# Performance work log

Hardware: AMD Instinct MI355X
Metric: run time of the kernel (lower is better)

The kernel has to match this reference:

```python
import jax, jax.numpy as jnp
import numpy as np

NUM_CLASSES = 21
TOP_K = 200
CONF_THRESH = 0.01
NMS_THRESH = 0.045
VAR0, VAR1 = 0.1, 0.2  # SSD decode variances
B, N = 128, 8732  # batch, num anchors (SSD300)


def setup_inputs() -> dict:
    key = jax.random.key(0)
    k1, k2, k3 = jax.random.split(key, 3)
    loc = jax.random.normal(k1, (B, N, 4), jnp.float32)
    conf = jax.random.normal(k2, (B, N, NUM_CLASSES), jnp.float32)
    # anchors in center-size form (cx, cy, w, h), values in (0,1)
    anchors = jax.random.uniform(k3, (N, 4), jnp.float32)
    return {"loc": loc, "conf": conf, "anchors": anchors}


def decode(loc, anchors):
    # loc [N,4], anchors [N,4] (cx,cy,w,h) -> corner boxes [N,4]
    cxcy = anchors[:, :2] + loc[:, :2] * VAR0 * anchors[:, 2:]
    wh = anchors[:, 2:] * jnp.exp(loc[:, 2:] * VAR1)
    return jnp.concatenate([cxcy - 0.5 * wh, cxcy + 0.5 * wh], axis=-1)


def pairwise_iou(boxes):
    # boxes [K,4] -> IoU [K,K]
    lt = jnp.maximum(boxes[:, None, :2], boxes[None, :, :2])
    rb = jnp.minimum(boxes[:, None, 2:], boxes[None, :, 2:])
    wh = jnp.clip(rb - lt, 0.0)
    inter = wh[..., 0] * wh[..., 1]
    area = (boxes[:, 2] - boxes[:, 0]) * (boxes[:, 3] - boxes[:, 1])
    return inter / (area[:, None] + area[None, :] - inter + 1e-12)


def nms_one_class(scores, boxes):
    # scores [N], boxes [N,4] -> packed [TOP_K, 5] (score, x1,y1,x2,y2)
    masked = jnp.where(scores > CONF_THRESH, scores, 0.0)
    top_s, idx = jax.lax.top_k(masked, TOP_K)
    top_b = boxes[idx]                      # [K,4]
    iou = pairwise_iou(top_b)               # [K,K]
    ar = jnp.arange(TOP_K)
    def body(i, keep):
        sup = keep[i] & (iou[i] > NMS_THRESH) & (ar > i)
        return keep & ~sup
    keep = jax.lax.fori_loop(0, TOP_K, body, top_s > CONF_THRESH)
    # pack kept detections to the front (stable sort preserves score order)
    order = jnp.argsort(jnp.logical_not(keep))
    ent = jnp.concatenate([top_s[:, None], top_b], axis=-1)[order]
    return jnp.where(keep[order][:, None], ent, 0.0)


def reference(loc, conf, anchors):
    probs = jax.nn.softmax(conf, axis=-1)   # [B,N,C]
    def per_image(loc_i, probs_i):
        boxes = decode(loc_i, anchors)      # [N,4]
        return jax.vmap(lambda s: nms_one_class(s, boxes))(probs_i.T)  # [C,K,5]
    out = jax.vmap(per_image)(loc, probs)   # [B,C,K,5]
    return out.at[:, 0].set(0.0)            # class 0 = background, left zero
```

## Files before the change

kernel.cpp:

```cpp
#include <hip/hip_runtime.h>
#include <math.h>

#pragma clang fp contract(off)

#define NB 128
#define NA 8732
#define NAP 8736
#define NC 21
#define TOPK 200
#define BCAP 512
#define CONF_T 0.01
#define NMS_T 0.045
#define NV (NAP / 8)
#define HSIZE 904
#define CHN 226
#define CHPAD 232
#define CH2N 29
#define KSAMP 30

__device__ __forceinline__ double exact_score_cf(const float* __restrict__ conf,
                                                 int b, int i, int c) {
  const float* row = conf + ((size_t)b * NA + i) * NC;
  float r[NC];
#pragma unroll
  for (int k = 0; k < NC; ++k) r[k] = row[k];
  float mx = r[0];
#pragma unroll
  for (int k = 1; k < NC; ++k) mx = fmaxf(mx, r[k]);
  double d = 0.0;
#pragma unroll
  for (int k = 0; k < NC; ++k) d += exp((double)r[k] - (double)mx);
  double s = exp((double)r[c] - (double)mx) / d;
  return (s > CONF_T) ? s : 0.0;
}

__device__ __forceinline__ double exact_score_aux(const float* __restrict__ conf,
                                                  const double2* __restrict__ aux,
                                                  int b, int i, int c) {
  size_t r = (size_t)b * NA + i;
  double v = (double)conf[r * NC + c];
  double2 a = aux[r];
  double s = exp(v - a.y) / a.x;
  return (s > CONF_T) ? s : 0.0;
}

__device__ __forceinline__ double exact_score(const float* __restrict__ conf,
                                              const double2* __restrict__ aux,
                                              int use_aux, int b, int i, int c) {
  if (use_aux) return exact_score_aux(conf, aux, b, i, c);
  return exact_score_cf(conf, b, i, c);
}

__device__ __forceinline__ void decode64(const float* __restrict__ loc,
                                         const float* __restrict__ anchors,
                                         int b, int ai, double* o) {
  const float* lp = loc + ((size_t)b * NA + ai) * 4;
  const float* ap = anchors + (size_t)ai * 4;
  double l0 = (double)lp[0], l1 = (double)lp[1];
  double l2 = (double)lp[2], l3 = (double)lp[3];
  double a0 = (double)ap[0], a1 = (double)ap[1];
  double a2 = (double)ap[2], a3 = (double)ap[3];
  double cx = a0 + (l0 * 0.1) * a2;
  double cy = a1 + (l1 * 0.1) * a3;
  double w = a2 * exp(l2 * 0.2);
  double h = a3 * exp(l3 * 0.2);
  o[0] = cx - 0.5 * w; o[1] = cy - 0.5 * h;
  o[2] = cx + 0.5 * w; o[3] = cy + 0.5 * h;
}

__device__ __forceinline__ bool entBefore(double sa, int ia, double sb, int ib) {
  return (sa > sb) || (sa == sb && ia < ib);
}

__device__ __forceinline__ unsigned wave_suffix_sum(unsigned v, int lane) {
#pragma unroll
  for (int off = 1; off < 64; off <<= 1) {
    unsigned o = (unsigned)__shfl_down((int)v, off);
    v += (lane + off < 64) ? o : 0u;
  }
  return v;
}

__global__ __launch_bounds__(256) void k_prep(const float* __restrict__ conf,
                                              unsigned short* __restrict__ scores,
                                              double2* __restrict__ aux,
                                              int do_aux) {
  __shared__ float rows[256 * NC];
  int base = blockIdx.x * 256;
  const float4* src = (const float4*)(conf + (size_t)base * NC);
  float4* dst = (float4*)rows;
  for (int t = threadIdx.x; t < (256 * NC) / 4; t += 256) dst[t] = src[t];
  __syncthreads();
  int g = base + threadIdx.x;
  const float* row = rows + threadIdx.x * NC;
  float v[NC];
#pragma unroll
  for (int k = 0; k < NC; ++k) v[k] = row[k];
  float mx = v[0];
#pragma unroll
  for (int k = 1; k < NC; ++k) mx = fmaxf(mx, v[k]);
  float e[NC], s = 0.0f;
#pragma unroll
  for (int k = 0; k < NC; ++k) {
    e[k] = expf(v[k] - mx);
    s += e[k];
  }
  float inv = 1.0f / s;
  int b = g / NA, i = g - b * NA;
#pragma unroll
  for (int cc = 1; cc < NC; ++cc) {
    float sc = e[cc] * inv;
    scores[(size_t)(b * (NC - 1) + (cc - 1)) * NAP + i] =
        (sc > 0.0099f) ? (unsigned short)(__float_as_uint(sc) >> 16)
                       : (unsigned short)0;
  }
  if (do_aux) {
    double d = 0.0;
#pragma unroll
    for (int k = 0; k < NC; ++k) d += exp((double)v[k] - (double)mx);
    aux[g] = make_double2(d, (double)mx);
  }
}

__global__ __launch_bounds__(256) void k_pad(unsigned short* __restrict__ scores,
                                             float* __restrict__ out) {
  int t = blockIdx.x * 256 + threadIdx.x;
  if (t < NB * TOPK * 5) {
    int bb = t / (TOPK * 5);
    int r = t - bb * (TOPK * 5);
    out[(size_t)bb * NC * TOPK * 5 + r] = 0.0f;
  }
  if (t < NB * (NC - 1)) {
    unsigned short* p = scores + (size_t)t * NAP + NA;
    p[0] = 0; p[1] = 0; p[2] = 0; p[3] = 0;
  }
}

__global__ __launch_bounds__(256, 8) void k_fast(const float* __restrict__ loc,
                                                 const float* __restrict__ conf,
                                                 const float* __restrict__ anchors,
                                                 const unsigned short* __restrict__ scores,
                                                 const double2* __restrict__ aux,
                                                 float* __restrict__ out,
                                                 int use_aux) {
  int id = blockIdx.x;
  int xcd = id & 7, slot0 = id >> 3;
  int c = 1 + (slot0 % (NC - 1));
  int b = (slot0 / (NC - 1)) * 8 + xcd;
  int tid = threadIdx.x;
  float* outbase = out + ((size_t)(b * NC + c)) * TOPK * 5;

  __shared__ unsigned hist[HSIZE];
  __shared__ unsigned chunk[CHPAD];
  __shared__ unsigned chunk2[32];
  union U2 {
    struct { double bnds[BCAP]; int bndi[BCAP]; } bb;
    double dbox[TOPK][4];
  };
  __shared__ U2 u2;
  union U3 {
    unsigned suf[HSIZE];
    struct { float4 fbox[TOPK]; float farea[TOPK]; } fb;
  };
  __shared__ U3 u3;
  __shared__ double ssel[256];
  __shared__ int isel[256];
  __shared__ unsigned keepw[7];
  __shared__ int ctl_cnt, ctl_m, ctl_n1, ctl_kneed, ctl_lo, ctl_hi, ctl_k;
  __shared__ int ctl_fix, ctl_redo;
  __shared__ unsigned ctl_pref, ctl_L;

  const unsigned short* srow =
      scores + (size_t)(b * (NC - 1) + (c - 1)) * NAP;
  const uint4* sv = (const uint4*)srow;

  for (int t = tid; t < TOPK; t += 256) isel[t] = 0;
  if (tid < 32) chunk2[tid] = 0u;
  if (tid == 0) { ctl_cnt = 0; ctl_m = 0; ctl_fix = 0; }
  __syncthreads();
  {
    unsigned k16 = srow[tid * 34];
    if (k16) {
      int x = (int)k16 - 0x3BFF;
      if (x < 1) x = 1;
      if (x > HSIZE - 1) x = HSIZE - 1;
      atomicAdd(&chunk2[x >> 5], 1u);
    }
  }
  __syncthreads();
  if (tid < 64) {
    unsigned h = (tid < CH2N) ? chunk2[tid] : 0u;
    unsigned s = wave_suffix_sum(h, tid);
    unsigned long long bal = __ballot((int)(tid < CH2N && s >= (unsigned)KSAMP));
    if (tid == 0) {
      int w = bal ? (63 - (int)__clzll(bal)) : -1;
      ctl_L = (w >= 1) ? (unsigned)(0x3BFF + (w << 5)) : 0u;
    }
  }
  __syncthreads();

  unsigned L16x = ctl_L ? ctl_L : 1u;
  int lo, hi, n1, kneed;
  for (;;) {
    for (int t = tid; t < HSIZE; t += 256) hist[t] = 0u;
    if (tid == 0) ctl_redo = 0;
    __syncthreads();
    for (int q = tid; q < NV; q += 256) {
      uint4 v = sv[q];
      unsigned ks[8] = {v.x & 0xFFFFu, v.x >> 16, v.y & 0xFFFFu, v.y >> 16,
                        v.z & 0xFFFFu, v.z >> 16, v.w & 0xFFFFu, v.w >> 16};
#pragma unroll
      for (int t = 0; t < 8; ++t) {
        if (ks[t] >= L16x) {
          int x = (int)ks[t] - 0x3BFF;
          if (x < 1) x = 1;
          if (x > HSIZE - 1) x = HSIZE - 1;
          atomicAdd(&hist[x], 1u);
        }
      }
    }
    __syncthreads();
    if (tid < CHN) {
      unsigned csum = 0;
#pragma unroll
      for (int j = 0; j < 4; ++j) csum += hist[tid * 4 + j];
      chunk[tid] = csum;
    } else if (tid < CHPAD) {
      chunk[tid] = 0u;
    }
    __syncthreads();
    if (tid < 64) {
      int lane = tid;
      unsigned h2 = 0;
      if (lane < CH2N) {
        int cb = lane * 8;
#pragma unroll
        for (int j = 0; j < 8; ++j) h2 += chunk[cb + j];
      }
      unsigned s2 = wave_suffix_sum(h2, lane);
      unsigned long long bal = __ballot((int)(lane < CH2N && s2 >= (unsigned)TOPK));
      int t2 = bal ? (63 - (int)__clzll(bal)) : -1;
      if (t2 < 0 && L16x > 1u) {
        if (lane == 0) ctl_redo = 1;
      } else {
        if (t2 < 0) {
          if (lane == 0) {
            ctl_lo = 1; ctl_hi = 0; ctl_n1 = (int)s2; ctl_kneed = TOPK - (int)s2;
          }
        } else {
          unsigned cumS = (unsigned)__shfl((int)(s2 - h2), t2);
          unsigned hc = (lane < 8) ? chunk[t2 * 8 + lane] : 0u;
          unsigned sc = wave_suffix_sum(hc, lane);
          unsigned long long balc =
              __ballot((int)(lane < 8 && cumS + sc >= (unsigned)TOPK));
          int jc = 63 - (int)__clzll(balc);
          int tc = t2 * 8 + jc;
          unsigned cumC = cumS + (unsigned)__shfl((int)(sc - hc), jc);
          unsigned hb = (lane < 4) ? hist[tc * 4 + lane] : 0u;
          unsigned sb = wave_suffix_sum(hb, lane);
          unsigned long long balb =
              __ballot((int)(lane < 4 && cumC + sb >= (unsigned)TOPK));
          int jb = 63 - (int)__clzll(balb);
          int D = tc * 4 + jb;
          unsigned cum = cumC + (unsigned)__shfl((int)(sb - hb), jb);
          int hi_ = (D + 1 < HSIZE) ? D + 1 : D;
          int lo_ = (D - 1 >= 1) ? D - 1 : D;
          unsigned hup = (hi_ > D) ? hist[hi_] : 0u;
          if (lane == 0) {
            ctl_lo = lo_; ctl_hi = hi_;
            ctl_n1 = (int)(cum - hup);
            ctl_kneed = TOPK - ctl_n1;
          }
        }
        if (lane < 32) chunk2[lane] = s2 - h2;
      }
    }
    __syncthreads();
    if (!ctl_redo) break;
    L16x = 1u;
  }
  lo = ctl_lo; hi = ctl_hi; n1 = ctl_n1; kneed = ctl_kneed;

  if (tid < CHN) {
    unsigned s = chunk2[tid >> 3];
    int ge = ((tid >> 3) + 1) << 3;
    for (int u = tid + 1; u < ge; ++u) s += chunk[u];
    int b0 = tid * 4;
    unsigned h3 = hist[b0 + 3], h2 = hist[b0 + 2], h1 = hist[b0 + 1];
    u3.suf[b0 + 3] = s;
    u3.suf[b0 + 2] = s + h3;
    u3.suf[b0 + 1] = s + h3 + h2;
    u3.suf[b0 + 0] = s + h3 + h2 + h1;
  }
  __syncthreads();

  {
    unsigned tC16 = (unsigned)(0x3C00 + hi);
    unsigned tB16 = (unsigned)(0x3BFF + lo);
    for (int q = tid; q < NV; q += 256) {
      uint4 v = sv[q];
      unsigned ks[8] = {v.x & 0xFFFFu, v.x >> 16, v.y & 0xFFFFu, v.y >> 16,
                        v.z & 0xFFFFu, v.z >> 16, v.w & 0xFFFFu, v.w >> 16};
#pragma unroll
      for (int t = 0; t < 8; ++t) {
        unsigned key = ks[t];
        if (key >= tC16) {
          int x = (int)key - 0x3BFF;
          if (x > HSIZE - 1) x = HSIZE - 1;
          int slot = (int)u3.suf[x] + (int)atomicSub(&hist[x], 1u) - 1;
          if (slot < TOPK) isel[slot] = (x << 16) | (q * 8 + t);
        } else if (key >= tB16) {
          int p = atomicAdd(&ctl_m, 1);
          if (p < BCAP) u2.bb.bndi[p] = q * 8 + t;
        }
      }
    }
  }
  __syncthreads();
  int m = (hi > 0) ? ctl_m : 0;

  if (hi > 0 && m > BCAP) {
    if (tid == 0) { ctl_k = TOPK; ctl_pref = 0u; }
    __syncthreads();
    for (int shift = 8; shift >= 0; shift -= 8) {
      hist[tid] = 0u;
      __syncthreads();
      unsigned pref = ctl_pref;
      for (int q = tid; q < NV; q += 256) {
        uint4 v = sv[q];
        unsigned ks[8] = {v.x & 0xFFFFu, v.x >> 16, v.y & 0xFFFFu, v.y >> 16,
                          v.z & 0xFFFFu, v.z >> 16, v.w & 0xFFFFu, v.w >> 16};
#pragma unroll
        for (int t = 0; t < 8; ++t) {
          unsigned key = ks[t];
          if (key == 0u) continue;
          bool match = (shift == 8) || ((key >> 8) == (pref >> 8));
          if (match) atomicAdd(&hist[(key >> shift) & 255u], 1u);
        }
      }
      __syncthreads();
      if (tid == 0) {
        int k = ctl_k;
        unsigned cum = 0;
        int d = 255;
        for (; d > 0; --d) {
          unsigned h = hist[d];
          if (cum + h >= (unsigned)k) break;
          cum += h;
        }
        ctl_k = k - (int)cum;
        ctl_pref = pref | ((unsigned)d << shift);
      }
      __syncthreads();
    }
    unsigned Tf = ctl_pref;
    kneed = ctl_k;
    n1 = TOPK - kneed;
    if (tid == 0) { ctl_cnt = 0; ctl_m = 0; }
    __syncthreads();
    for (int q = tid; q < NV; q += 256) {
      uint4 v = sv[q];
      unsigned ks[8] = {v.x & 0xFFFFu, v.x >> 16, v.y & 0xFFFFu, v.y >> 16,
                        v.z & 0xFFFFu, v.z >> 16, v.w & 0xFFFFu, v.w >> 16};
#pragma unroll
      for (int t = 0; t < 8; ++t) {
        unsigned key = ks[t];
        if (key > Tf) {
          int p = atomicAdd(&ctl_cnt, 1);
          if (p < 256) isel[p] = q * 8 + t;
        } else if (key == Tf) {
          int p = atomicAdd(&ctl_m, 1);
          if (p < BCAP) u2.bb.bndi[p] = q * 8 + t;
        }
      }
    }
    __syncthreads();
    m = ctl_m;
    if (m > BCAP) m = BCAP;
    for (int q = tid; q < m; q += 256)
      u2.bb.bnds[q] = exact_score(conf, aux, use_aux, b, u2.bb.bndi[q], c);
    __syncthreads();
    for (int q = tid; q < m; q += 256) {
      double sq = u2.bb.bnds[q];
      int iq = u2.bb.bndi[q];
      int rank = 0;
      for (int r = 0; r < m; ++r)
        if (entBefore(u2.bb.bnds[r], u2.bb.bndi[r], sq, iq)) ++rank;
      if (rank < kneed) { isel[n1 + rank] = iq; ssel[n1 + rank] = sq; }
    }
    __syncthreads();
    if (tid < TOPK) {
      if (tid < n1) ssel[tid] = exact_score(conf, aux, use_aux, b, isel[tid], c);
    } else {
      ssel[tid] = -1.0;
      isel[tid] = 0x7fffffff;
    }
    for (int kk = 2; kk <= 256; kk <<= 1) {
      for (int j = kk >> 1; j > 0; j >>= 1) {
        __syncthreads();
        int ixj = tid ^ j;
        if (ixj > tid) {
          double s1 = ssel[tid], s2 = ssel[ixj];
          int i1 = isel[tid], i2 = isel[ixj];
          bool up = ((tid & kk) == 0);
          bool sw = up ? entBefore(s2, i2, s1, i1) : entBefore(s1, i1, s2, i2);
          if (sw) {
            ssel[tid] = s2; ssel[ixj] = s1;
            isel[tid] = i2; isel[ixj] = i1;
          }
        }
      }
    }
    __syncthreads();
  } else {
    if (tid < n1)
      ssel[tid] = exact_score(conf, aux, use_aux, b, isel[tid] & 0xFFFF, c);
    if (hi > 0) {
      for (int q = tid; q < m; q += 256)
        u2.bb.bnds[q] = exact_score(conf, aux, use_aux, b, u2.bb.bndi[q], c);
    }
    __syncthreads();
    double myS = 0.0;
    int myI = 0, myPos = -1;
    if (tid < n1) {
      int packed = isel[tid];
      int bk = packed >> 16;
      myI = packed & 0xFFFF;
      myS = ssel[tid];
      int base = (int)u3.suf[bk];
      int len = (int)u3.suf[bk - 1] - base;
      int r = 0;
      for (int u = base; u < base + len; ++u) {
        if (u == tid) continue;
        double ps = ssel[u];
        int pI = isel[u] & 0xFFFF;
        if (entBefore(ps, pI, myS, myI)) ++r;
      }
      myPos = base + r;
    }
    if (hi > 0) {
      for (int q = tid; q < m; q += 256) {
        double sq = u2.bb.bnds[q];
        int iq = u2.bb.bndi[q];
        int rank = 0;
        for (int r = 0; r < m; ++r)
          if (entBefore(u2.bb.bnds[r], u2.bb.bndi[r], sq, iq)) ++rank;
        if (rank < kneed) { isel[n1 + rank] = iq; ssel[n1 + rank] = sq; }
      }
    } else {
      for (int j = n1 + tid; j < TOPK; j += 256) {
        isel[j] = j - n1;
        ssel[j] = 0.0;
      }
    }
    __syncthreads();
    if (myPos >= 0 && myPos < TOPK) { ssel[myPos] = myS; isel[myPos] = myI; }
    __syncthreads();
    if (tid < 64) {
      bool inv = false;
      for (int j = tid + 1; j < TOPK; j += 64)
        if (entBefore(ssel[j], isel[j], ssel[j - 1], isel[j - 1])) inv = true;
      unsigned long long bal = __ballot((int)inv);
      if (tid == 0 && bal != 0ull) ctl_fix = 1;
    }
    __syncthreads();
    if (ctl_fix) {
      if (tid == 0) {
        for (int a = 1; a < TOPK; ++a) {
          double s = ssel[a];
          int ii = isel[a];
          int p = a - 1;
          while (p >= 0 && entBefore(s, ii, ssel[p], isel[p])) {
            ssel[p + 1] = ssel[p]; isel[p + 1] = isel[p]; --p;
          }
          ssel[p + 1] = s; isel[p + 1] = ii;
        }
      }
      __syncthreads();
    }
  }

  float fx1 = 0, fy1 = 0, fx2 = 0, fy2 = 0;
  if (tid < TOPK) {
    int ai = isel[tid];
    const float* lp = loc + ((size_t)b * NA + ai) * 4;
    const float* ap = anchors + (size_t)ai * 4;
    float l0 = lp[0], l1 = lp[1], l2 = lp[2], l3 = lp[3];
    float a0 = ap[0], a1 = ap[1], a2 = ap[2], a3 = ap[3];
    float cx = a0 + (l0 * 0.1f) * a2;
    float cy = a1 + (l1 * 0.1f) * a3;
    float w = a2 * expf(l2 * 0.2f);
    float h = a3 * expf(l3 * 0.2f);
    fx1 = cx - 0.5f * w; fy1 = cy - 0.5f * h;
    fx2 = cx + 0.5f * w; fy2 = cy + 0.5f * h;
    u3.fb.fbox[tid] = make_float4(fx1, fy1, fx2, fy2);
    u3.fb.farea[tid] = (fx2 - fx1) * (fy2 - fy1);
    double dcx = (double)a0 + ((double)l0 * 0.1) * (double)a2;
    double dcy = (double)a1 + ((double)l1 * 0.1) * (double)a3;
    double dw = (double)a2 * exp((double)l2 * 0.2);
    double dh = (double)a3 * exp((double)l3 * 0.2);
    u2.dbox[tid][0] = dcx - 0.5 * dw;
    u2.dbox[tid][1] = dcy - 0.5 * dh;
    u2.dbox[tid][2] = dcx + 0.5 * dw;
    u2.dbox[tid][3] = dcy + 0.5 * dh;
  }
  __syncthreads();

  if (tid < 64) {
    int l = tid;
    unsigned kr = 0u;
    float4 ob[4]; float oa[4];
#pragma unroll
    for (int q = 0; q < 4; ++q) {
      int j = l + 64 * q;
      if (j < TOPK) {
        if (ssel[j] > CONF_T) kr |= 1u << q;
        ob[q] = u3.fb.fbox[j];
        oa[q] = u3.fb.farea[j];
      } else {
        ob[q] = make_float4(0.0f, 0.0f, 0.0f, 0.0f);
        oa[q] = 0.0f;
      }
    }
    int cur = 0;
    while (cur < TOPK) {
      unsigned long long ms0 = __ballot((int)(kr & 1u));
      unsigned long long ms1 = __ballot((int)(kr & 2u));
      unsigned long long ms2 = __ballot((int)(kr & 4u));
      unsigned long long ms3 = __ballot((int)(kr & 8u));
      int q0 = cur >> 6;
      int sh = cur & 63;
      unsigned long long below = sh ? ((1ull << sh) - 1ull) : 0ull;
      unsigned long long t0 = (q0 == 0) ? (ms0 & ~below) : 0ull;
      unsigned long long t1 = (q0 < 1) ? ms1 : ((q0 == 1) ? (ms1 & ~below) : 0ull);
      unsigned long long t2 = (q0 < 2) ? ms2 : ((q0 == 2) ? (ms2 & ~below) : 0ull);
      unsigned long long t3 = (q0 < 3) ? ms3 : (ms3 & ~below);
      int i = TOPK;
      if (t0) i = __ffsll(t0) - 1;
      else if (t1) i = 64 + __ffsll(t1) - 1;
      else if (t2) i = 128 + __ffsll(t2) - 1;
      else if (t3) i = 192 + __ffsll(t3) - 1;
      if (i >= TOPK) break;
      float4 fbi = u3.fb.fbox[i];
      float fai = u3.fb.farea[i];
#pragma unroll
      for (int q = 0; q < 4; ++q) {
        int r = l + 64 * q;
        if (r > i && r < TOPK && ((kr >> q) & 1u)) {
          float lx = fmaxf(fbi.x, ob[q].x), ly = fmaxf(fbi.y, ob[q].y);
          float rx = fminf(fbi.z, ob[q].z), ry = fminf(fbi.w, ob[q].w);
          float iw = fmaxf(rx - lx, 0.0f), ih = fmaxf(ry - ly, 0.0f);
          float inter = iw * ih;
          float uni = fai + oa[q] - inter + 1e-12f;
          float diff = inter - 0.045f * uni;
          bool sup;
          if (fabsf(diff) < 3e-4f * uni) {
            double ix1 = u2.dbox[i][0], iy1 = u2.dbox[i][1];
            double ix2 = u2.dbox[i][2], iy2 = u2.dbox[i][3];
            double jx1 = u2.dbox[r][0], jy1 = u2.dbox[r][1];
            double jx2 = u2.dbox[r][2], jy2 = u2.dbox[r][3];
            double dlx = fmax(ix1, jx1), dly = fmax(iy1, jy1);
            double drx = fmin(ix2, jx2), dry = fmin(iy2, jy2);
            double diw = drx - dlx; if (diw < 0.0) diw = 0.0;
            double dih = dry - dly; if (dih < 0.0) dih = 0.0;
            double dint = diw * dih;
            double dai = (ix2 - ix1) * (iy2 - iy1);
            double daj = (jx2 - jx1) * (jy2 - jy1);
            sup = dint > NMS_T * (dai + daj - dint + 1e-12);
          } else {
            sup = diff > 0.0f;
          }
          if (sup) kr &= ~(1u << q);
        }
      }
      cur = i + 1;
    }
#pragma unroll
    for (int q = 0; q < 4; ++q) {
      unsigned long long bal = __ballot((int)((kr >> q) & 1u));
      if (l == 0) {
        keepw[2 * q] = (unsigned)bal;
        if (2 * q + 1 < 7) keepw[2 * q + 1] = (unsigned)(bal >> 32);
      }
    }
  }
  __syncthreads();

  int nk = 0;
#pragma unroll
  for (int w = 0; w < 7; ++w) nk += __popc(keepw[w]);
  if (tid < TOPK) {
    int j = tid;
    bool kept = (keepw[j >> 5] >> (j & 31)) & 1u;
    if (kept) {
      int pos = 0;
      for (int w = 0; w < (j >> 5); ++w) pos += __popc(keepw[w]);
      pos += __popc(keepw[j >> 5] & ((1u << (j & 31)) - 1u));
      float* o = outbase + (size_t)pos * 5;
      o[0] = (float)ssel[j];
      o[1] = fx1;
      o[2] = fy1;
      o[3] = fx2;
      o[4] = fy2;
    }
    if (j >= nk) {
      float* o = outbase + (size_t)j * 5;
      o[0] = 0.0f; o[1] = 0.0f; o[2] = 0.0f; o[3] = 0.0f; o[4] = 0.0f;
    }
  }
}

__global__ __launch_bounds__(256) void k_main_nf(const float* __restrict__ loc,
                                                 const float* __restrict__ conf,
                                                 const float* __restrict__ anchors,
                                                 float* __restrict__ out) {
  int bc = blockIdx.x;
  int b = bc / NC;
  int c = bc % NC;
  int tid = threadIdx.x;
  float* outbase = out + (size_t)bc * TOPK * 5;
  if (c == 0) {
    for (int k = tid; k < TOPK * 5; k += 256) outbase[k] = 0.0f;
    return;
  }
  union U {
    float sf[NA];
    struct { double box[TOPK][4]; double area[TOPK]; } p2;
  };
  __shared__ U u;
  __shared__ double ssel[256];
  __shared__ int isel[256];
  __shared__ unsigned hist[256];
  __shared__ double bnds[256];
  __shared__ int bndi[256];
  __shared__ int keepL[256];
  __shared__ unsigned long long wmask[4];
  __shared__ int ctl_k, ctl_cnt, ctl_m;
  __shared__ unsigned ctl_pref;

  for (int i = tid; i < NA; i += 256)
    u.sf[i] = (float)exact_score_cf(conf, b, i, c);
  if (tid == 0) { ctl_k = TOPK; ctl_pref = 0u; }
  __syncthreads();
  for (int shift = 24; shift >= 0; shift -= 8) {
    hist[tid] = 0u;
    __syncthreads();
    unsigned pref = ctl_pref;
    for (int i = tid; i < NA; i += 256) {
      unsigned key = __float_as_uint(u.sf[i]);
      bool match = (shift == 24) || ((key >> (shift + 8)) == (pref >> (shift + 8)));
      if (match) atomicAdd(&hist[(key >> shift) & 255u], 1u);
    }
    __syncthreads();
    if (tid == 0) {
      int k = ctl_k;
      unsigned cum = 0;
      int d = 255;
      for (; d > 0; --d) {
        unsigned h = hist[d];
        if (cum + h >= (unsigned)k) break;
        cum += h;
      }
      ctl_k = k - (int)cum;
      ctl_pref = pref | ((unsigned)d << shift);
    }
    __syncthreads();
  }
  unsigned Tf = ctl_pref;
  int kneed = ctl_k;
  int n1 = TOPK - kneed;
  if (tid == 0) { ctl_cnt = 0; ctl_m = 0; }
  __syncthreads();
  for (int i = tid; i < NA; i += 256) {
    unsigned key = __float_as_uint(u.sf[i]);
    if (key > Tf) {
      int p = atomicAdd(&ctl_cnt, 1);
      if (p < 256) isel[p] = i;
    } else if (key == Tf && Tf != 0u) {
      int q = atomicAdd(&ctl_m, 1);
      if (q < 256) bndi[q] = i;
    }
  }
  __syncthreads();
  int zf;
  if (Tf == 0u) {
    zf = n1;
    for (int j = n1 + tid; j < TOPK; j += 256) isel[j] = j - n1;
  } else {
    zf = TOPK;
    int m = ctl_m;
    if (m > 256) m = 256;
    if (tid < m) bnds[tid] = exact_score_cf(conf, b, bndi[tid], c);
    __syncthreads();
    if (tid < m) {
      double sq = bnds[tid];
      int iq = bndi[tid];
      int rank = 0;
      for (int r = 0; r < m; ++r)
        if (entBefore(bnds[r], bndi[r], sq, iq)) ++rank;
      if (rank < kneed) isel[n1 + rank] = iq;
    }
  }
  __syncthreads();
  if (tid < TOPK) {
    ssel[tid] = (tid < zf) ? exact_score_cf(conf, b, isel[tid], c) : 0.0;
  } else {
    ssel[tid] = -1.0;
    isel[tid] = 0x7fffffff;
  }
  for (int kk = 2; kk <= 256; kk <<= 1) {
    for (int j = kk >> 1; j > 0; j >>= 1) {
      __syncthreads();
      int ixj = tid ^ j;
      if (ixj > tid) {
        double s1 = ssel[tid], s2 = ssel[ixj];
        int i1 = isel[tid], i2 = isel[ixj];
        bool up = ((tid & kk) == 0);
        bool sw = up ? entBefore(s2, i2, s1, i1) : entBefore(s1, i1, s2, i2);
        if (sw) {
          ssel[tid] = s2; ssel[ixj] = s1;
          isel[tid] = i2; isel[ixj] = i1;
        }
      }
    }
  }
  __syncthreads();
  if (tid < TOPK) {
    double bx[4];
    decode64(loc, anchors, b, isel[tid], bx);
    u.p2.box[tid][0] = bx[0]; u.p2.box[tid][1] = bx[1];
    u.p2.box[tid][2] = bx[2]; u.p2.box[tid][3] = bx[3];
    u.p2.area[tid] = (bx[2] - bx[0]) * (bx[3] - bx[1]);
  }
  __syncthreads();
  double mx1 = 0, my1 = 0, mx2 = 0, my2 = 0, mar = 0;
  if (tid < TOPK) {
    mx1 = u.p2.box[tid][0]; my1 = u.p2.box[tid][1];
    mx2 = u.p2.box[tid][2]; my2 = u.p2.box[tid][3];
    mar = u.p2.area[tid];
  }
  keepL[tid] = (tid < TOPK) && (ssel[tid] > CONF_T);
  __syncthreads();
  for (int i = 0; i < TOPK; ++i) {
    int ki = keepL[i];
    if (ki && tid > i && tid < TOPK && keepL[tid]) {
      double lx = fmax(u.p2.box[i][0], mx1);
      double ly = fmax(u.p2.box[i][1], my1);
      double rx = fmin(u.p2.box[i][2], mx2);
      double ry = fmin(u.p2.box[i][3], my2);
      double iw = rx - lx; if (iw < 0.0) iw = 0.0;
      double ih = ry - ly; if (ih < 0.0) ih = 0.0;
      double inter = iw * ih;
      double iou = inter / (u.p2.area[i] + mar - inter + 1e-12);
      if (iou > NMS_T) keepL[tid] = 0;
    }
    __syncthreads();
  }
  bool kj = (tid < TOPK) && (keepL[tid] != 0);
  unsigned long long bal = __ballot((int)kj);
  int wave = tid >> 6, lane = tid & 63;
  if (lane == 0) wmask[wave] = bal;
  __syncthreads();
  int nk = 0;
#pragma unroll
  for (int w = 0; w < 4; ++w) nk += __popcll(wmask[w]);
  if (kj) {
    int pos = 0;
    for (int w = 0; w < wave; ++w) pos += __popcll(wmask[w]);
    pos += __popcll(bal & ((1ull << lane) - 1ull));
    float* o = outbase + (size_t)pos * 5;
    o[0] = (float)ssel[tid];
    o[1] = (float)u.p2.box[tid][0];
    o[2] = (float)u.p2.box[tid][1];
    o[3] = (float)u.p2.box[tid][2];
    o[4] = (float)u.p2.box[tid][3];
  }
  if (tid < TOPK && tid >= nk) {
    float* o = outbase + (size_t)tid * 5;
    o[0] = 0.0f; o[1] = 0.0f; o[2] = 0.0f; o[3] = 0.0f; o[4] = 0.0f;
  }
}

extern "C" void kernel_launch(void* const* d_in, const int* in_sizes, int n_in,
                              void* d_out, int out_size, void* d_ws, size_t ws_size,
                              hipStream_t stream) {
  const float* loc = (const float*)d_in[0];
  const float* conf = (const float*)d_in[1];
  const float* anchors = (const float*)d_in[2];
  float* out = (float*)d_out;

  const size_t SC_BYTES = (size_t)NB * (NC - 1) * NAP * sizeof(unsigned short);
  const size_t AUX_BYTES = (size_t)NB * NA * sizeof(double2);

  if (ws_size >= SC_BYTES + AUX_BYTES) {
    unsigned short* scores = (unsigned short*)d_ws;
    double2* aux = (double2*)((char*)d_ws + SC_BYTES);
    k_pad<<<(NB * TOPK * 5 + 255) / 256, 256, 0, stream>>>(scores, out);
    k_prep<<<(NB * NA) / 256, 256, 0, stream>>>(conf, scores, aux, 1);
    k_fast<<<NB * (NC - 1), 256, 0, stream>>>(loc, conf, anchors, scores, aux, out, 1);
  } else if (ws_size >= SC_BYTES) {
    unsigned short* scores = (unsigned short*)d_ws;
    k_pad<<<(NB * TOPK * 5 + 255) / 256, 256, 0, stream>>>(scores, out);
    k_prep<<<(NB * NA) / 256, 256, 0, stream>>>(conf, scores, nullptr, 0);
    k_fast<<<NB * (NC - 1), 256, 0, stream>>>(loc, conf, anchors, scores, nullptr, out, 0);
  } else {
    k_main_nf<<<NB * NC, 256, 0, stream>>>(loc, conf, anchors, out);
  }
}
```

Before: 115.6 us.

## Build exact coarse score histogram in prep kernel to set tight prefilter threshold

The prep kernel now accumulates a per-image, per-class 32-bucket histogram of score keys in shared memory and flushes it to global memory with atomics. The NMS kernel reads this exact histogram instead of sampling 256 scores, and picks a threshold guaranteeing at least TOPK candidates. Most scores then fall below the threshold and skip the fine-histogram atomics. The cost is extra shared and global atomics in prep, plus a zeroing pass in the pad kernel. Clamping of histogram indices was also removed, which depends on the threshold always keeping keys in range.

```diff
diff --git a/kernel.cpp b/kernel.cpp
--- a/kernel.cpp
+++ b/kernel.cpp
@@ -16,7 +16,7 @@
 #define CHN 226
 #define CHPAD 232
 #define CH2N 29
-#define KSAMP 30
+#define SHN ((NC - 1) * 32)
 
 __device__ __forceinline__ double exact_score_cf(const float* __restrict__ conf,
                                                  int b, int i, int c) {
@@ -84,12 +84,15 @@
 __global__ __launch_bounds__(256) void k_prep(const float* __restrict__ conf,
                                               unsigned short* __restrict__ scores,
                                               double2* __restrict__ aux,
+                                              unsigned* __restrict__ shist,
                                               int do_aux) {
   __shared__ float rows[256 * NC];
+  __shared__ unsigned sh[2 * SHN];
   int base = blockIdx.x * 256;
   const float4* src = (const float4*)(conf + (size_t)base * NC);
   float4* dst = (float4*)rows;
   for (int t = threadIdx.x; t < (256 * NC) / 4; t += 256) dst[t] = src[t];
+  for (int t = threadIdx.x; t < 2 * SHN; t += 256) sh[t] = 0u;
   __syncthreads();
   int g = base + threadIdx.x;
   const float* row = rows + threadIdx.x * NC;
@@ -107,12 +110,17 @@
   }
   float inv = 1.0f / s;
   int b = g / NA, i = g - b * NA;
+  int b_first = base / NA;
+  int dz = (b - b_first) * SHN;
 #pragma unroll
   for (int cc = 1; cc < NC; ++cc) {
     float sc = e[cc] * inv;
-    scores[(size_t)(b * (NC - 1) + (cc - 1)) * NAP + i] =
+    unsigned short key =
         (sc > 0.0099f) ? (unsigned short)(__float_as_uint(sc) >> 16)
                        : (unsigned short)0;
+    scores[(size_t)(b * (NC - 1) + (cc - 1)) * NAP + i] = key;
+    if (key)
+      atomicAdd(&sh[dz + (cc - 1) * 32 + (((int)key - 0x3BFF) >> 5)], 1u);
   }
   if (do_aux) {
     double d = 0.0;
@@ -120,10 +128,20 @@
     for (int k = 0; k < NC; ++k) d += exp((double)v[k] - (double)mx);
     aux[g] = make_double2(d, (double)mx);
   }
+  __syncthreads();
+  for (int t = threadIdx.x; t < 2 * SHN; t += 256) {
+    unsigned cnt = sh[t];
+    if (cnt) {
+      int d0 = t / SHN;
+      int rem = t - d0 * SHN;
+      atomicAdd(&shist[(size_t)(b_first + d0) * SHN + rem], cnt);
+    }
+  }
 }
 
 __global__ __launch_bounds__(256) void k_pad(unsigned short* __restrict__ scores,
-                                             float* __restrict__ out) {
+                                             float* __restrict__ out,
+                                             unsigned* __restrict__ shist) {
   int t = blockIdx.x * 256 + threadIdx.x;
   if (t < NB * TOPK * 5) {
     int bb = t / (TOPK * 5);
@@ -134,6 +152,7 @@
     unsigned short* p = scores + (size_t)t * NAP + NA;
     p[0] = 0; p[1] = 0; p[2] = 0; p[3] = 0;
   }
+  if (t < NB * SHN) shist[t] = 0u;
 }
 
 __global__ __launch_bounds__(256, 8) void k_fast(const float* __restrict__ loc,
@@ -141,6 +160,7 @@
                                                  const float* __restrict__ anchors,
                                                  const unsigned short* __restrict__ scores,
                                                  const double2* __restrict__ aux,
+                                                 const unsigned* __restrict__ shist,
                                                  float* __restrict__ out,
                                                  int use_aux) {
   int id = blockIdx.x;
@@ -175,23 +195,12 @@
   const uint4* sv = (const uint4*)srow;
 
   for (int t = tid; t < TOPK; t += 256) isel[t] = 0;
-  if (tid < 32) chunk2[tid] = 0u;
   if (tid == 0) { ctl_cnt = 0; ctl_m = 0; ctl_fix = 0; }
-  __syncthreads();
-  {
-    unsigned k16 = srow[tid * 34];
-    if (k16) {
-      int x = (int)k16 - 0x3BFF;
-      if (x < 1) x = 1;
-      if (x > HSIZE - 1) x = HSIZE - 1;
-      atomicAdd(&chunk2[x >> 5], 1u);
-    }
-  }
-  __syncthreads();
   if (tid < 64) {
-    unsigned h = (tid < CH2N) ? chunk2[tid] : 0u;
+    const unsigned* shrow = shist + (size_t)(b * (NC - 1) + (c - 1)) * 32;
+    unsigned h = (tid < 32) ? shrow[tid] : 0u;
     unsigned s = wave_suffix_sum(h, tid);
-    unsigned long long bal = __ballot((int)(tid < CH2N && s >= (unsigned)KSAMP));
+    unsigned long long bal = __ballot((int)(tid < 32 && s >= (unsigned)TOPK));
     if (tid == 0) {
       int w = bal ? (63 - (int)__clzll(bal)) : -1;
       ctl_L = (w >= 1) ? (unsigned)(0x3BFF + (w << 5)) : 0u;
@@ -211,12 +220,7 @@
                         v.z & 0xFFFFu, v.z >> 16, v.w & 0xFFFFu, v.w >> 16};
 #pragma unroll
       for (int t = 0; t < 8; ++t) {
-        if (ks[t] >= L16x) {
-          int x = (int)ks[t] - 0x3BFF;
-          if (x < 1) x = 1;
-          if (x > HSIZE - 1) x = HSIZE - 1;
-          atomicAdd(&hist[x], 1u);
-        }
+        if (ks[t] >= L16x) atomicAdd(&hist[(int)ks[t] - 0x3BFF], 1u);
       }
     }
     __syncthreads();
@@ -257,7 +261,7 @@
           int tc = t2 * 8 + jc;
           unsigned cumC = cumS + (unsigned)__shfl((int)(sc - hc), jc);
           unsigned hb = (lane < 4) ? hist[tc * 4 + lane] : 0u;
-          unsigned sb = wave_suffix_sum(hb, lane);
+      unsigned sb = wave_suffix_sum(hb, lane);
           unsigned long long balb =
               __ballot((int)(lane < 4 && cumC + sb >= (unsigned)TOPK));
           int jb = 63 - (int)__clzll(balb);
@@ -306,7 +310,6 @@
         unsigned key = ks[t];
         if (key >= tC16) {
           int x = (int)key - 0x3BFF;
-          if (x > HSIZE - 1) x = HSIZE - 1;
           int slot = (int)u3.suf[x] + (int)atomicSub(&hist[x], 1u) - 1;
           if (slot < TOPK) isel[slot] = (x << 16) | (q * 8 + t);
         } else if (key >= tB16) {
@@ -791,18 +794,23 @@
 
   const size_t SC_BYTES = (size_t)NB * (NC - 1) * NAP * sizeof(unsigned short);
   const size_t AUX_BYTES = (size_t)NB * NA * sizeof(double2);
-
-  if (ws_size >= SC_BYTES + AUX_BYTES) {
+  const size_t SH_BYTES = (size_t)NB * SHN * sizeof(unsigned);
+
+  int padGrid = (NB * TOPK * 5 + 255) / 256;
+
+  if (ws_size >= SC_BYTES + AUX_BYTES + SH_BYTES) {
     unsigned short* scores = (unsigned short*)d_ws;
     double2* aux = (double2*)((char*)d_ws + SC_BYTES);
-    k_pad<<<(NB * TOPK * 5 + 255) / 256, 256, 0, stream>>>(scores, out);
-    k_prep<<<(NB * NA) / 256, 256, 0, stream>>>(conf, scores, aux, 1);
-    k_fast<<<NB * (NC - 1), 256, 0, stream>>>(loc, conf, anchors, scores, aux, out, 1);
-  } else if (ws_size >= SC_BYTES) {
+    unsigned* shist = (unsigned*)((char*)d_ws + SC_BYTES + AUX_BYTES);
+    k_pad<<<padGrid, 256, 0, stream>>>(scores, out, shist);
+    k_prep<<<(NB * NA) / 256, 256, 0, stream>>>(conf, scores, aux, shist, 1);
+    k_fast<<<NB * (NC - 1), 256, 0, stream>>>(loc, conf, anchors, scores, aux, shist, out, 1);
+  } else if (ws_size >= SC_BYTES + SH_BYTES) {
     unsigned short* scores = (unsigned short*)d_ws;
-    k_pad<<<(NB * TOPK * 5 + 255) / 256, 256, 0, stream>>>(scores, out);
-    k_prep<<<(NB * NA) / 256, 256, 0, stream>>>(conf, scores, nullptr, 0);
-    k_fast<<<NB * (NC - 1), 256, 0, stream>>>(loc, conf, anchors, scores, nullptr, out, 0);
+    unsigned* shist = (unsigned*)((char*)d_ws + SC_BYTES);
+    k_pad<<<padGrid, 256, 0, stream>>>(scores, out, shist);
+    k_prep<<<(NB * NA) / 256, 256, 0, stream>>>(conf, scores, nullptr, shist, 0);
+    k_fast<<<NB * (NC - 1), 256, 0, stream>>>(loc, conf, anchors, scores, nullptr, shist, out, 0);
   } else {
     k_main_nf<<<NB * NC, 256, 0, stream>>>(loc, conf, anchors, out);
   }
```

New measurement: 119.8 us. 1.04x slower.
